# Kernel optimization log

Measured on AMD Instinct MI355X. Metric: run time of the kernel, lower is better.

The kernel has to match this reference:

```python
import jax, jax.numpy as jnp
import numpy as np

D_FEAT = 6
HID = 256
T = 60
B_DAYS = 4
STOCKS = 512
TRAIN_DAYS = 240
K_DAY = 10
N_NEIGHBOR = 10
SLOPE = 0.01  # nn.LeakyReLU default


def setup_inputs() -> dict:
    key = jax.random.key(0)
    ks = jax.random.split(key, 32)
    g = lambda i, shape, s=0.05: (jax.random.normal(ks[i], shape, dtype=jnp.float32) * s)
    inp = jax.random.normal(ks[0], (B_DAYS, STOCKS, D_FEAT * T), dtype=jnp.float32)
    train_hidden = jax.random.normal(ks[1], (TRAIN_DAYS, STOCKS, HID), dtype=jnp.float32)
    train_hidden_day = jax.random.normal(ks[2], (TRAIN_DAYS, HID), dtype=jnp.float32)
    return {
        "inp": inp,
        "train_hidden": train_hidden,
        "train_hidden_day": train_hidden_day,
        # GRU layer 0 (input D_FEAT) and layer 1 (input HID); gates [r,z,n] stacked -> 3*HID
        "W_ih0": g(3, (3 * HID, D_FEAT)), "W_hh0": g(4, (3 * HID, HID)),
        "b_ih0": g(5, (3 * HID,)), "b_hh0": g(6, (3 * HID,)),
        "W_ih1": g(7, (3 * HID, HID)), "W_hh1": g(8, (3 * HID, HID)),
        "b_ih1": g(9, (3 * HID,)), "b_hh1": g(10, (3 * HID,)),
        # lins MLP 256->512->512->256
        "lin0_W": g(11, (512, HID)), "lin0_b": g(12, (512,)),
        "lin1_W": g(13, (512, 512)), "lin1_b": g(14, (512,)),
        "lin2_W": g(15, (HID, 512)), "lin2_b": g(16, (HID,)),
        # projections (no bias) and output head
        "proj1_W": g(17, (HID, HID)), "proj2_W": g(18, (HID, HID)),
        "fc_W": g(19, (1, 2 * HID)), "fc_b": g(20, (1,)),
    }


def _leaky(x):
    return jnp.where(x >= 0, x, SLOPE * x)


def _gru_layer(x, W_ih, W_hh, b_ih, b_hh):
    # x: [N, T, in] -> [N, T, HID]
    xW = jnp.einsum('nti,gi->ntg', x, W_ih) + b_ih  # precompute input gates
    def step(h, xw):
        gh = h @ W_hh.T + b_hh
        xr, xz, xn = jnp.split(xw, 3, axis=-1)
        hr, hz, hn = jnp.split(gh, 3, axis=-1)
        r = jax.nn.sigmoid(xr + hr)
        z = jax.nn.sigmoid(xz + hz)
        n = jnp.tanh(xn + r * hn)
        h = (1.0 - z) * n + z * h
        return h, h
    h0 = jnp.zeros((x.shape[0], W_hh.shape[1]), x.dtype)
    _, hs = jax.lax.scan(step, h0, jnp.swapaxes(xW, 0, 1))
    return jnp.swapaxes(hs, 0, 1)


def _cos_sim(x, y):
    xy = x @ y.T
    xn = jnp.sqrt(jnp.sum(x * x, axis=1))[:, None]
    yn = jnp.sqrt(jnp.sum(y * y, axis=1))[:, None]
    cs = xy / (xn @ yn.T)
    return jnp.where(jnp.isnan(cs), 0.0, cs)


def reference(inp, train_hidden, train_hidden_day,
              W_ih0, W_hh0, b_ih0, b_hh0, W_ih1, W_hh1, b_ih1, b_hh1,
              lin0_W, lin0_b, lin1_W, lin1_b, lin2_W, lin2_b,
              proj1_W, proj2_W, fc_W, fc_b):
    B, S = inp.shape[0], inp.shape[1]
    x = inp.reshape(B * S, D_FEAT, -1).transpose(0, 2, 1)  # [N, T, d_feat]
    h = _gru_layer(x, W_ih0, W_hh0, b_ih0, b_hh0)
    h = _gru_layer(h, W_ih1, W_hh1, b_ih1, b_hh1)
    out = h[:, -1, :]                                      # [N, HID]
    mb = _leaky(out @ lin0_W.T + lin0_b)
    mb = _leaky(mb @ lin1_W.T + lin1_b)
    mb = _leaky(mb @ lin2_W.T + lin2_b)                    # mini_batch_out [N, HID]
    mb_day = jnp.mean(mb.reshape(B, S, -1), axis=1)        # [B, HID]
    day_sim = _cos_sim(mb_day, train_hidden_day)           # [B, TRAIN_DAYS]
    _, day_idx = jax.lax.top_k(day_sim, K_DAY)             # [B, K_DAY]
    sample = train_hidden[day_idx].reshape(-1, train_hidden.shape[-1])  # [B*K_DAY*S, HID]
    q = mb @ proj1_W.T
    kh = sample @ proj2_W.T
    cs = _cos_sim(q, kh)                                   # [N, B*K_DAY*S]
    vals, idx = jax.lax.top_k(cs, N_NEIGHBOR)              # per-row top-k (distinct cols)
    # sparse mask (ones/n_neighbor) * cos_sim, then sparse @ kh == weighted gather-sum
    agg = jnp.einsum('nk,nkh->nh', vals / N_NEIGHBOR, kh[idx])
    cat = jnp.concatenate([mb, agg], axis=1)               # [N, 2*HID]
    y = (cat @ fc_W.T + fc_b).squeeze(-1)
    return y.reshape(B, -1)
```

## Files before the change

### kernel.cpp

```cpp
#include <hip/hip_runtime.h>
#include <cmath>
#include <cstdint>

#define D_FEAT 6
#define T_SEQ  60
#define HID    256
#define G3     768
#define NROW   2048
#define NSAMP  20480

__device__ __forceinline__ float sigmoidf_(float x) { return 1.0f / (1.0f + expf(-x)); }

struct PrepArgs {
  const float* src[9];
  float* dst[9];
  int N[9], K[9], ro[9];
};

__global__ void prep_weights(PrepArgs a) {
  int seg = blockIdx.y;
  const float* S = a.src[seg];
  float* D = a.dst[seg];
  int N = a.N[seg], K = a.K[seg], ro = a.ro[seg];
  int total = N * K;
  for (int i = blockIdx.x * blockDim.x + threadIdx.x; i < total; i += gridDim.x * blockDim.x) {
    int n = i / K, k = i - n * K;
    D[(size_t)(k + ro) * N + n] = S[i];
  }
}

__device__ __forceinline__ void kloop128(const float* __restrict__ A,
                                         const float* __restrict__ B,
                                         float (&acc)[3][8])
{
  float4 Aa[4][2];
  float  Bb[2][12];
#pragma unroll
  for (int c = 0; c < 4; ++c) {
    Aa[c][0] = *(const float4*)(A + c * 8);
    Aa[c][1] = *(const float4*)(A + c * 8 + 4);
  }
#pragma unroll
  for (int c = 0; c < 4; ++c)
#pragma unroll
    for (int u = 0; u < 3; ++u)
      Bb[0][c * 3 + u] = B[(size_t)c * G3 + u * 256];

  for (int kb = 0; kb < 128; kb += 8) {
    {
      const float* p = B + (size_t)(kb + 4) * G3;
#pragma unroll
      for (int c = 0; c < 4; ++c)
#pragma unroll
        for (int u = 0; u < 3; ++u)
          Bb[1][c * 3 + u] = p[(size_t)c * G3 + u * 256];
    }
#pragma unroll
    for (int c = 0; c < 4; ++c) {
      float4 alo = Aa[c][0], ahi = Aa[c][1];
      int kn = kb + 4 + c;
      Aa[c][0] = *(const float4*)(A + kn * 8);
      Aa[c][1] = *(const float4*)(A + kn * 8 + 4);
#pragma unroll
      for (int u = 0; u < 3; ++u) {
        float b = Bb[0][c * 3 + u];
        acc[u][0] += alo.x * b; acc[u][1] += alo.y * b;
        acc[u][2] += alo.z * b; acc[u][3] += alo.w * b;
        acc[u][4] += ahi.x * b; acc[u][5] += ahi.y * b;
        acc[u][6] += ahi.z * b; acc[u][7] += ahi.w * b;
      }
    }
    {
      int kw = (kb + 8) & 127;
      const float* p = B + (size_t)kw * G3;
#pragma unroll
      for (int c = 0; c < 4; ++c)
#pragma unroll
        for (int u = 0; u < 3; ++u)
          Bb[0][c * 3 + u] = p[(size_t)c * G3 + u * 256];
    }
#pragma unroll
    for (int c = 0; c < 4; ++c) {
      float4 alo = Aa[c][0], ahi = Aa[c][1];
      int kn = (kb + 8 + c) & 127;
      Aa[c][0] = *(const float4*)(A + kn * 8);
      Aa[c][1] = *(const float4*)(A + kn * 8 + 4);
#pragma unroll
      for (int u = 0; u < 3; ++u) {
        float b = Bb[1][c * 3 + u];
        acc[u][0] += alo.x * b; acc[u][1] += alo.y * b;
        acc[u][2] += alo.z * b; acc[u][3] += alo.w * b;
        acc[u][4] += ahi.x * b; acc[u][5] += ahi.y * b;
        acc[u][6] += ahi.z * b; acc[u][7] += ahi.w * b;
      }
    }
  }
}

__global__ __launch_bounds__(512, 1)
void gru_fused(const float* __restrict__ inp, const float* __restrict__ WThh0,
               const float* __restrict__ WTcat, const float* __restrict__ WTih0,
               const float* __restrict__ bih0, const float* __restrict__ bhh0,
               const float* __restrict__ bih1, const float* __restrict__ bhh1,
               float* __restrict__ hrow)
{
  __shared__ float h0A[2048], h0B[2048];
  __shared__ float h1A[2048], h1B[2048];
  __shared__ float xls[2880];
  __shared__ float exch[256 * 33];

  const int tid = threadIdx.x;
  const int col = tid & 255;
  const int half = tid >> 8;
  const int m0 = blockIdx.x * 8;

  for (int c = tid; c < 2880; c += 512) {
    int row = c / 360, it = c - row * 360;
    xls[it * 8 + row] = inp[(size_t)(m0 + row) * 360 + it];
  }
  for (int c = tid; c < 2048; c += 512) { h0A[c] = 0.f; h1A[c] = 0.f; }

  float h0c[8], h1c[8];
#pragma unroll
  for (int r = 0; r < 8; ++r) { h0c[r] = 0.f; h1c[r] = 0.f; }

  float b_ih0[3], b_hh0[3], b_ih1[3], b_hh1[3];
#pragma unroll
  for (int u = 0; u < 3; ++u) {
    int o = u * 256 + col;
    b_ih0[u] = bih0[o]; b_hh0[u] = bhh0[o];
    b_ih1[u] = bih1[o]; b_hh1[u] = bhh1[o];
  }
  __syncthreads();

  const int aoff = half * 1024;
  const float* Bhh0 = WThh0 + (size_t)(half * 128) * G3 + col;
  const float* Bc0  = WTcat + (size_t)(half * 128) * G3 + col;
  const float* Bc1  = WTcat + (size_t)(256 + half * 128) * G3 + col;
  float* exc = exch + col * 33;

  for (int t = 0; t < T_SEQ; ++t) {
    const float* h0cur = (t & 1) ? h0B : h0A;
    float*       h0nxt = (t & 1) ? h0A : h0B;
    const float* h1cur = (t & 1) ? h1B : h1A;
    float*       h1nxt = (t & 1) ? h1A : h1B;

    float gh[3][8];
#pragma unroll
    for (int u = 0; u < 3; ++u)
#pragma unroll
      for (int r = 0; r < 8; ++r) gh[u][r] = 0.f;
    kloop128(h0cur + aoff, Bhh0, gh);

    float xw[3][8];
    if (half == 0) {
#pragma unroll
      for (int u = 0; u < 3; ++u)
#pragma unroll
        for (int r = 0; r < 8; ++r) xw[u][r] = b_ih0[u];
#pragma unroll
      for (int i = 0; i < 6; ++i) {
        float4 xlo = *(const float4*)&xls[(i * 60 + t) * 8];
        float4 xhi = *(const float4*)&xls[(i * 60 + t) * 8 + 4];
#pragma unroll
        for (int u = 0; u < 3; ++u) {
          float b = WTih0[i * G3 + u * 256 + col];
          xw[u][0] += xlo.x * b; xw[u][1] += xlo.y * b;
          xw[u][2] += xlo.z * b; xw[u][3] += xlo.w * b;
          xw[u][4] += xhi.x * b; xw[u][5] += xhi.y * b;
          xw[u][6] += xhi.z * b; xw[u][7] += xhi.w * b;
        }
      }
    } else {
#pragma unroll
      for (int u = 0; u < 3; ++u)
#pragma unroll
        for (int r = 0; r < 8; ++r) exc[u * 8 + r] = gh[u][r];
    }
    __syncthreads();

    if (half == 0) {
      float hn[8];
#pragma unroll
      for (int r = 0; r < 8; ++r) {
        float g0 = gh[0][r] + exc[r];
        float g1 = gh[1][r] + exc[8 + r];
        float g2 = gh[2][r] + exc[16 + r];
        float rr = sigmoidf_(xw[0][r] + (g0 + b_hh0[0]));
        float zz = sigmoidf_(xw[1][r] + (g1 + b_hh0[1]));
        float nn = tanhf(xw[2][r] + rr * (g2 + b_hh0[2]));
        h0c[r] = (1.f - zz) * nn + zz * h0c[r];
        hn[r] = h0c[r];
      }
      *(float4*)&h0nxt[col * 8]     = *(float4*)&hn[0];
      *(float4*)&h0nxt[col * 8 + 4] = *(float4*)&hn[4];
    }
    __syncthreads();

    float acc[3][8];
#pragma unroll
    for (int u = 0; u < 3; ++u)
#pragma unroll
      for (int r = 0; r < 8; ++r) acc[u][r] = 0.f;
    kloop128(h0nxt + aoff, Bc0, acc);
    float xn8[8];
#pragma unroll
    for (int r = 0; r < 8; ++r) { xn8[r] = acc[2][r]; acc[2][r] = 0.f; }
    kloop128(h1cur + aoff, Bc1, acc);

    if (half == 1) {
#pragma unroll
      for (int r = 0; r < 8; ++r) {
        exc[r]      = acc[0][r];
        exc[8 + r]  = acc[1][r];
        exc[16 + r] = xn8[r];
        exc[24 + r] = acc[2][r];
      }
    }
    __syncthreads();

    if (half == 0) {
      float hn[8];
#pragma unroll
      for (int r = 0; r < 8; ++r) {
        float ra = acc[0][r] + exc[r];
        float za = acc[1][r] + exc[8 + r];
        float xa = xn8[r] + exc[16 + r];
        float ha = acc[2][r] + exc[24 + r];
        float rr = sigmoidf_((ra + b_ih1[0]) + b_hh1[0]);
        float zz = sigmoidf_((za + b_ih1[1]) + b_hh1[1]);
        float nn = tanhf((xa + b_ih1[2]) + rr * (ha + b_hh1[2]));
        h1c[r] = (1.f - zz) * nn + zz * h1c[r];
        hn[r] = h1c[r];
      }
      *(float4*)&h1nxt[col * 8]     = *(float4*)&hn[0];
      *(float4*)&h1nxt[col * 8 + 4] = *(float4*)&hn[4];
    }
    __syncthreads();
  }

  if (half == 0) {
#pragma unroll
    for (int r = 0; r < 8; ++r)
      hrow[(size_t)(m0 + r) * 256 + col] = h1c[r];
  }
}

__global__ __launch_bounds__(256, 2)
void gemm_act(const float* __restrict__ A, const int* __restrict__ rowsrc,
              const float* __restrict__ WT, const float* __restrict__ bias,
              float* __restrict__ C, int M, int N, int K, int act)
{
  __shared__ float4 As4[128 * 32];
  const int tx = threadIdx.x, ty = threadIdx.y;
  const int tid = ty * 32 + tx;
  const int n0 = blockIdx.x * 32, m0 = blockIdx.y * 32;
  const int K4 = K >> 2;

  for (int c = tid; c < K4 * 32; c += 256) {
    int k4 = c % K4, m = c / K4;
    int row = m0 + m;
    if (rowsrc) row = rowsrc[row];
    As4[k4 * 32 + m] = *(const float4*)(A + (size_t)row * K + k4 * 4);
  }
  __syncthreads();

  float acc[4] = {0,0,0,0};
  const int n = n0 + tx;
  const float* pb = WT + n;

  float bc[4], bn_[4];
#pragma unroll
  for (int kk = 0; kk < 4; ++kk) bc[kk] = pb[(size_t)kk * N];
  for (int k4 = 0; k4 < K4; ++k4) {
    int nk4 = (k4 + 1 < K4) ? (k4 + 1) : 0;
    const float* pn = pb + (size_t)nk4 * 4 * N;
#pragma unroll
    for (int kk = 0; kk < 4; ++kk) bn_[kk] = pn[(size_t)kk * N];
    float4 a0 = As4[k4 * 32 + ty * 4 + 0];
    float4 a1 = As4[k4 * 32 + ty * 4 + 1];
    float4 a2 = As4[k4 * 32 + ty * 4 + 2];
    float4 a3 = As4[k4 * 32 + ty * 4 + 3];
#pragma unroll
    for (int kk = 0; kk < 4; ++kk) {
      float b = bc[kk];
      acc[0] += ((const float*)&a0)[kk] * b;
      acc[1] += ((const float*)&a1)[kk] * b;
      acc[2] += ((const float*)&a2)[kk] * b;
      acc[3] += ((const float*)&a3)[kk] * b;
    }
#pragma unroll
    for (int q = 0; q < 4; ++q) bc[q] = bn_[q];
  }
  float bb = bias ? bias[n] : 0.f;
#pragma unroll
  for (int r = 0; r < 4; ++r) {
    float v = acc[r] + bb;
    if (act) v = (v >= 0.f) ? v : 0.01f * v;
    C[(size_t)(m0 + ty * 4 + r) * N + n] = v;
  }
}

__global__ void mbday_part(const float* __restrict__ mbf, float* __restrict__ part) {
  int d = blockIdx.x, sl = blockIdx.y, c = threadIdx.x;
  float s = 0.f;
  int base = d * 512 + sl * 64;
  for (int st = 0; st < 64; ++st) s += mbf[(size_t)(base + st) * 256 + c];
  part[(size_t)(d * 8 + sl) * 256 + c] = s;
}

__global__ void mbday_fin(const float* __restrict__ part, float* __restrict__ mbday) {
  int d = blockIdx.x, c = threadIdx.x;
  float s = 0.f;
#pragma unroll
  for (int p = 0; p < 8; ++p) s += part[(size_t)(d * 8 + p) * 256 + c];
  mbday[d * 256 + c] = s * (1.0f / 512.0f);
}

__global__ void daytopk_kernel(const float* __restrict__ mbday, const float* __restrict__ thd,
                               int* __restrict__ dayidx) {
  __shared__ float mbs[256];
  __shared__ float sim[256];
  __shared__ float red[256];
  __shared__ int   redi[256];
  const int d = blockIdx.x, t = threadIdx.x;
  mbs[t] = mbday[d * 256 + t];
  __syncthreads();
  red[t] = mbs[t] * mbs[t];
  __syncthreads();
  for (int o = 128; o; o >>= 1) { if (t < o) red[t] += red[t + o]; __syncthreads(); }
  float xn = sqrtf(red[0]);
  float v = -INFINITY;
  if (t < 240) {
    float dot = 0.f, yn2 = 0.f;
    for (int k = 0; k < 256; ++k) {
      float y = thd[t * 256 + k];
      dot += mbs[k] * y;
      yn2 += y * y;
    }
    float den = xn * sqrtf(yn2);
    v = (den > 0.f) ? dot / den : 0.f;
  }
  sim[t] = v;
  __syncthreads();
  for (int it = 0; it < 10; ++it) {
    red[t] = sim[t]; redi[t] = t;
    __syncthreads();
    for (int o = 128; o; o >>= 1) {
      if (t < o) {
        if (red[t + o] > red[t] || (red[t + o] == red[t] && redi[t + o] < redi[t])) {
          red[t] = red[t + o]; redi[t] = redi[t + o];
        }
      }
      __syncthreads();
    }
    if (t == 0) { int bi = redi[0]; dayidx[d * 10 + it] = bi; sim[bi] = -INFINITY; }
    __syncthreads();
  }
}

__global__ void rowsrc_kernel(const int* __restrict__ dayidx, int* __restrict__ rowsrc) {
  int r = blockIdx.x * 256 + threadIdx.x;
  if (r < NSAMP) rowsrc[r] = dayidx[r >> 9] * 512 + (r & 511);
}

__global__ void rownorm_kernel(const float* __restrict__ X, float* __restrict__ out, int rows) {
  int w = threadIdx.x >> 6;
  int lane = threadIdx.x & 63;
  int row = blockIdx.x * 4 + w;
  if (row >= rows) return;
  float4 x = *(const float4*)(X + (size_t)row * 256 + lane * 4);
  float s = x.x * x.x + x.y * x.y + x.z * x.z + x.w * x.w;
#pragma unroll
  for (int o = 32; o; o >>= 1) s += __shfl_down(s, o, 64);
  if (lane == 0) out[row] = sqrtf(s);
}

__global__ void qnorm_kernel(float* __restrict__ q, const float* __restrict__ qn) {
  int i = blockIdx.x * 256 + threadIdx.x;
  int row = i >> 8;
  float n = qn[row];
  q[i] = (n > 0.f) ? q[i] / n : 0.f;
}

__global__ void khT_kernel(const float* __restrict__ kh, const float* __restrict__ khn,
                           float* __restrict__ khT) {
  __shared__ float tile[32][33];
  int jb = blockIdx.x * 32;
  int kb = blockIdx.y * 32;
  int tx = threadIdx.x & 31, tyy = threadIdx.x >> 5;
  for (int rr = tyy; rr < 32; rr += 8) {
    float n = khn[jb + rr];
    float v = kh[(size_t)(jb + rr) * 256 + kb + tx];
    tile[rr][tx] = (n > 0.f) ? v / n : 0.f;
  }
  __syncthreads();
  for (int rr = tyy; rr < 32; rr += 8) {
    khT[(size_t)(kb + rr) * NSAMP + jb + tx] = tile[tx][rr];
  }
}

__global__ __launch_bounds__(256, 4)
void csmax_kernel(const float* __restrict__ qh, const float* __restrict__ khT,
                  float* __restrict__ topvp, int* __restrict__ topip)
{
  __shared__ float4 qs[256][2];
  __shared__ float csch[8 * 512];
  const int tid = threadIdx.x;
  const int split = blockIdx.x & 7;
  const int m0 = (blockIdx.x >> 3) * 8;
  {
    int k = tid;
    float4 v0, v1;
    v0.x = qh[(size_t)(m0 + 0) * 256 + k]; v0.y = qh[(size_t)(m0 + 1) * 256 + k];
    v0.z = qh[(size_t)(m0 + 2) * 256 + k]; v0.w = qh[(size_t)(m0 + 3) * 256 + k];
    v1.x = qh[(size_t)(m0 + 4) * 256 + k]; v1.y = qh[(size_t)(m0 + 5) * 256 + k];
    v1.z = qh[(size_t)(m0 + 6) * 256 + k]; v1.w = qh[(size_t)(m0 + 7) * 256 + k];
    qs[k][0] = v0; qs[k][1] = v1;
  }
  __syncthreads();
  const int lane = tid & 63;
  const int wv = tid >> 6;

  float tv0[10], tv1[10];
  int   tj0[10], tj1[10];
  int   tn0 = 0, tn1 = 0;
  float tmv0 = -INFINITY, tmv1 = -INFINITY;
  int   tmi0 = 0, tmi1 = 0;

  auto process_row = [&](int r, float (&tv)[10], int (&tj)[10], int& tn,
                         float& tmv, int& tmi, int jb) {
    float4 c0 = *(const float4*)&csch[r * 512 + lane * 8];
    float4 c1 = *(const float4*)&csch[r * 512 + lane * 8 + 4];
    float cv[8] = {c0.x, c0.y, c0.z, c0.w, c1.x, c1.y, c1.z, c1.w};
    const int cj0 = jb + lane * 8;
    while (true) {
      float bv = -INFINITY; int bj = 0x7fffffff;
#pragma unroll
      for (int u = 0; u < 8; ++u) {
        if (cv[u] > bv) { bv = cv[u]; bj = cj0 + u; }
      }
#pragma unroll
      for (int o = 32; o; o >>= 1) {
        float ov = __shfl_down(bv, o, 64);
        int   oj = __shfl_down(bj, o, 64);
        if (ov > bv || (ov == bv && oj < bj)) { bv = ov; bj = oj; }
      }
      bv = __shfl(bv, 0, 64); bj = __shfl(bj, 0, 64);
      bool take;
      if (tn < 10) take = true;
      else take = (bv > tmv) || (bv == tmv && bj < tmi);
      if (!take) break;
      if (tn < 10) {
#pragma unroll
        for (int s = 0; s < 10; ++s) if (s == tn) { tv[s] = bv; tj[s] = bj; }
        tn++;
        if (tn == 10) {
          float mv = tv[0]; int mi = tj[0];
#pragma unroll
          for (int s = 1; s < 10; ++s) {
            bool w = (tv[s] < mv) || (tv[s] == mv && tj[s] > mi);
            if (w) { mv = tv[s]; mi = tj[s]; }
          }
          tmv = mv; tmi = mi;
        }
      } else {
        int ms = 0; float mv = tv[0]; int mi = tj[0];
#pragma unroll
        for (int s = 1; s < 10; ++s) {
          bool w = (tv[s] < mv) || (tv[s] == mv && tj[s] > mi);
          if (w) { ms = s; mv = tv[s]; mi = tj[s]; }
        }
#pragma unroll
        for (int s = 0; s < 10; ++s) if (s == ms) { tv[s] = bv; tj[s] = bj; }
        mv = tv[0]; mi = tj[0];
#pragma unroll
        for (int s = 1; s < 10; ++s) {
          bool w = (tv[s] < mv) || (tv[s] == mv && tj[s] > mi);
          if (w) { mv = tv[s]; mi = tj[s]; }
        }
        tmv = mv; tmi = mi;
      }
#pragma unroll
      for (int u = 0; u < 8; ++u) if (cj0 + u == bj) cv[u] = -INFINITY;
    }
  };

  for (int ci = 0; ci < 5; ++ci) {
    const int ch = split * 5 + ci;
    const int jb = ch * 512;
    float acc[8][2];
#pragma unroll
    for (int r = 0; r < 8; ++r) { acc[r][0] = 0.f; acc[r][1] = 0.f; }
    const float* kp = khT + jb + tid;

    float b0c[4], b1c[4], b0n[4], b1n[4];
#pragma unroll
    for (int kk = 0; kk < 4; ++kk) {
      b0c[kk] = kp[(size_t)kk * NSAMP];
      b1c[kk] = kp[(size_t)kk * NSAMP + 256];
    }
    for (int k4 = 0; k4 < 64; ++k4) {
      int nk4 = (k4 + 1) & 63;
      const float* pn = kp + (size_t)nk4 * 4 * NSAMP;
#pragma unroll
      for (int kk = 0; kk < 4; ++kk) {
        b0n[kk] = pn[(size_t)kk * NSAMP];
        b1n[kk] = pn[(size_t)kk * NSAMP + 256];
      }
#pragma unroll
      for (int kk = 0; kk < 4; ++kk) {
        float4 qa = qs[k4 * 4 + kk][0];
        float4 qb = qs[k4 * 4 + kk][1];
        float b0 = b0c[kk], b1 = b1c[kk];
        acc[0][0] += qa.x * b0; acc[1][0] += qa.y * b0; acc[2][0] += qa.z * b0; acc[3][0] += qa.w * b0;
        acc[4][0] += qb.x * b0; acc[5][0] += qb.y * b0; acc[6][0] += qb.z * b0; acc[7][0] += qb.w * b0;
        acc[0][1] += qa.x * b1; acc[1][1] += qa.y * b1; acc[2][1] += qa.z * b1; acc[3][1] += qa.w * b1;
        acc[4][1] += qb.x * b1; acc[5][1] += qb.y * b1; acc[6][1] += qb.z * b1; acc[7][1] += qb.w * b1;
      }
#pragma unroll
      for (int q = 0; q < 4; ++q) { b0c[q] = b0n[q]; b1c[q] = b1n[q]; }
    }
    __syncthreads();
#pragma unroll
    for (int r = 0; r < 8; ++r) {
      csch[r * 512 + tid] = acc[r][0];
      csch[r * 512 + 256 + tid] = acc[r][1];
    }
    __syncthreads();
    process_row(wv,     tv0, tj0, tn0, tmv0, tmi0, jb);
    process_row(wv + 4, tv1, tj1, tn1, tmv1, tmi1, jb);
  }
  __syncthreads();

  if (lane == 0) {
    int row0 = m0 + wv;
#pragma unroll
    for (int s = 0; s < 10; ++s) {
      topvp[(size_t)row0 * 80 + split * 10 + s] = tv0[s];
      topip[(size_t)row0 * 80 + split * 10 + s] = tj0[s];
    }
    int row1 = m0 + wv + 4;
#pragma unroll
    for (int s = 0; s < 10; ++s) {
      topvp[(size_t)row1 * 80 + split * 10 + s] = tv1[s];
      topip[(size_t)row1 * 80 + split * 10 + s] = tj1[s];
    }
  }
}

__global__ void merge_topk(const float* __restrict__ topvp, const int* __restrict__ topip,
                           float* __restrict__ topv, int* __restrict__ topi)
{
  const int wv = threadIdx.x >> 6;
  const int lane = threadIdx.x & 63;
  const int row = blockIdx.x * 4 + wv;
  float v0 = topvp[(size_t)row * 80 + lane];
  int   i0 = topip[(size_t)row * 80 + lane];
  float v1 = (lane < 16) ? topvp[(size_t)row * 80 + 64 + lane] : -INFINITY;
  int   i1 = (lane < 16) ? topip[(size_t)row * 80 + 64 + lane] : 0x7fffffff;
  for (int s = 0; s < 10; ++s) {
    float bv = v0; int bj = i0;
    if (v1 > bv || (v1 == bv && i1 < bj)) { bv = v1; bj = i1; }
#pragma unroll
    for (int o = 1; o < 64; o <<= 1) {
      float ov = __shfl_xor(bv, o, 64);
      int   oj = __shfl_xor(bj, o, 64);
      if (ov > bv || (ov == bv && oj < bj)) { bv = ov; bj = oj; }
    }
    if (lane == 0) { topv[row * 10 + s] = bv; topi[row * 10 + s] = bj; }
    if (i0 == bj) { v0 = -INFINITY; i0 = 0x7fffffff; }
    if (i1 == bj) { v1 = -INFINITY; i1 = 0x7fffffff; }
  }
}

__global__ void final_kernel(const float* __restrict__ mb, const float* __restrict__ kh,
                             const float* __restrict__ topv, const int* __restrict__ topi,
                             const float* __restrict__ fcW, const float* __restrict__ fcb,
                             float* __restrict__ y)
{
  __shared__ float red[256];
  int n = blockIdx.x, c = threadIdx.x;
  float agg = 0.f;
#pragma unroll
  for (int k = 0; k < 10; ++k) {
    float w = topv[n * 10 + k] / 10.0f;
    int idx = topi[n * 10 + k];
    agg += w * kh[(size_t)idx * 256 + c];
  }
  float val = fcW[c] * mb[(size_t)n * 256 + c] + fcW[256 + c] * agg;
  red[c] = val;
  __syncthreads();
  for (int o = 128; o; o >>= 1) { if (c < o) red[c] += red[c + o]; __syncthreads(); }
  if (c == 0) y[n] = red[0] + fcb[0];
}

extern "C" void kernel_launch(void* const* d_in, const int* in_sizes, int n_in,
                              void* d_out, int out_size, void* d_ws, size_t ws_size,
                              hipStream_t stream)
{
  const float* inp    = (const float*)d_in[0];
  const float* trainh = (const float*)d_in[1];
  const float* thd    = (const float*)d_in[2];
  const float* Wih0   = (const float*)d_in[3];
  const float* Whh0   = (const float*)d_in[4];
  const float* bih0   = (const float*)d_in[5];
  const float* bhh0   = (const float*)d_in[6];
  const float* Wih1   = (const float*)d_in[7];
  const float* Whh1   = (const float*)d_in[8];
  const float* bih1   = (const float*)d_in[9];
  const float* bhh1   = (const float*)d_in[10];
  const float* lin0W  = (const float*)d_in[11];
  const float* lin0b  = (const float*)d_in[12];
  const float* lin1W  = (const float*)d_in[13];
  const float* lin1b  = (const float*)d_in[14];
  const float* lin2W  = (const float*)d_in[15];
  const float* lin2b  = (const float*)d_in[16];
  const float* p1W    = (const float*)d_in[17];
  const float* p2W    = (const float*)d_in[18];
  const float* fcW    = (const float*)d_in[19];
  const float* fcb    = (const float*)d_in[20];

  float* ws = (float*)d_ws;
  float* WT_hh0 = ws + 0;
  float* WTcat  = ws + 196608;
  float* WT_l0  = ws + 589824;
  float* WT_l1  = ws + 720896;
  float* WT_l2  = ws + 983040;
  float* WT_p1  = ws + 1114112;
  float* WT_p2  = ws + 1179648;
  float* hrow   = ws + 1245184;
  float* mb1    = ws + 3342336;
  float* mb2    = ws + 4390912;
  float* mbf    = ws + 5439488;
  float* mbday  = ws + 5963776;
  float* qbuf   = ws + 5964800;
  float* kh     = ws + 6489088;
  float* khT    = ws + 11731968;
  float* khn    = ws + 16974848;
  float* qn     = ws + 16995328;
  float* topv   = ws + 16997376;
  int*   dayidx = (int*)(ws + 17017856);
  int*   rowsrc = (int*)(ws + 17017920);
  int*   topi   = (int*)(ws + 17038400);
  float* topvp  = mb1;
  int*   topip  = (int*)(mb1 + 163840);
  float* WT_ih0 = mb2;
  float* mbpart = mb2;

  PrepArgs pa;
  pa.src[0] = Whh0;  pa.dst[0] = WT_hh0; pa.N[0] = 768; pa.K[0] = 256; pa.ro[0] = 0;
  pa.src[1] = Wih1;  pa.dst[1] = WTcat;  pa.N[1] = 768; pa.K[1] = 256; pa.ro[1] = 0;
  pa.src[2] = Whh1;  pa.dst[2] = WTcat;  pa.N[2] = 768; pa.K[2] = 256; pa.ro[2] = 256;
  pa.src[3] = lin0W; pa.dst[3] = WT_l0;  pa.N[3] = 512; pa.K[3] = 256; pa.ro[3] = 0;
  pa.src[4] = lin1W; pa.dst[4] = WT_l1;  pa.N[4] = 512; pa.K[4] = 512; pa.ro[4] = 0;
  pa.src[5] = lin2W; pa.dst[5] = WT_l2;  pa.N[5] = 256; pa.K[5] = 512; pa.ro[5] = 0;
  pa.src[6] = p1W;   pa.dst[6] = WT_p1;  pa.N[6] = 256; pa.K[6] = 256; pa.ro[6] = 0;
  pa.src[7] = p2W;   pa.dst[7] = WT_p2;  pa.N[7] = 256; pa.K[7] = 256; pa.ro[7] = 0;
  pa.src[8] = Wih0;  pa.dst[8] = WT_ih0; pa.N[8] = 768; pa.K[8] = 6;   pa.ro[8] = 0;
  prep_weights<<<dim3(64, 9), dim3(256), 0, stream>>>(pa);

  gru_fused<<<256, 512, 0, stream>>>(inp, WT_hh0, WTcat, WT_ih0, bih0, bhh0, bih1, bhh1, hrow);

  gemm_act<<<dim3(16, 64), dim3(32, 8), 0, stream>>>(hrow, nullptr, WT_l0, lin0b, mb1, 2048, 512, 256, 1);
  gemm_act<<<dim3(16, 64), dim3(32, 8), 0, stream>>>(mb1, nullptr, WT_l1, lin1b, mb2, 2048, 512, 512, 1);
  gemm_act<<<dim3(8, 64),  dim3(32, 8), 0, stream>>>(mb2, nullptr, WT_l2, lin2b, mbf, 2048, 256, 512, 1);

  mbday_part<<<dim3(4, 8), 256, 0, stream>>>(mbf, mbpart);
  mbday_fin<<<4, 256, 0, stream>>>(mbpart, mbday);
  daytopk_kernel<<<4, 256, 0, stream>>>(mbday, thd, dayidx);
  rowsrc_kernel<<<80, 256, 0, stream>>>(dayidx, rowsrc);

  gemm_act<<<dim3(8, 640), dim3(32, 8), 0, stream>>>(trainh, rowsrc, WT_p2, nullptr, kh, 20480, 256, 256, 0);
  gemm_act<<<dim3(8, 64),  dim3(32, 8), 0, stream>>>(mbf, nullptr, WT_p1, nullptr, qbuf, 2048, 256, 256, 0);

  rownorm_kernel<<<5120, 256, 0, stream>>>(kh, khn, 20480);
  rownorm_kernel<<<512, 256, 0, stream>>>(qbuf, qn, 2048);
  qnorm_kernel<<<2048, 256, 0, stream>>>(qbuf, qn);
  khT_kernel<<<dim3(640, 8), 256, 0, stream>>>(kh, khn, khT);

  csmax_kernel<<<2048, 256, 0, stream>>>(qbuf, khT, topvp, topip);
  merge_topk<<<512, 256, 0, stream>>>(topvp, topip, topv, topi);
  final_kernel<<<2048, 256, 0, stream>>>(mbf, kh, topv, topi, fcW, fcb, (float*)d_out);

  (void)in_sizes; (void)n_in; (void)out_size; (void)ws_size;
}
```

Before: 3.283 ms.

## Pipeline GRU layers across timesteps and split rows over 1024 threads

The fused two-layer GRU kernel now runs layer 0 at step p and layer 1 at step p-1 in the same phase. This drops one of the two barriers per step and lets all three k-loops run concurrently. The block grows to 1024 threads, with each thread covering 4 rows instead of 8, so per-thread registers drop and more waves are available to hide latency. The cost is that each weight column is read twice per block from global memory/cache, and there is one extra pipeline step at the end.

```diff
diff --git a/kernel.cpp b/kernel.cpp
--- a/kernel.cpp
+++ b/kernel.cpp
@@ -29,17 +29,14 @@
   }
 }
 
-__device__ __forceinline__ void kloop128(const float* __restrict__ A,
-                                         const float* __restrict__ B,
-                                         float (&acc)[3][8])
+__device__ __forceinline__ void kloop128q(const float* __restrict__ A,
+                                          const float* __restrict__ B,
+                                          float (&acc)[3][4])
 {
-  float4 Aa[4][2];
+  float4 Aa[4];
   float  Bb[2][12];
 #pragma unroll
-  for (int c = 0; c < 4; ++c) {
-    Aa[c][0] = *(const float4*)(A + c * 8);
-    Aa[c][1] = *(const float4*)(A + c * 8 + 4);
-  }
+  for (int c = 0; c < 4; ++c) Aa[c] = *(const float4*)(A + c * 8);
 #pragma unroll
   for (int c = 0; c < 4; ++c)
 #pragma unroll
@@ -57,17 +54,14 @@
     }
 #pragma unroll
     for (int c = 0; c < 4; ++c) {
-      float4 alo = Aa[c][0], ahi = Aa[c][1];
+      float4 a = Aa[c];
       int kn = kb + 4 + c;
-      Aa[c][0] = *(const float4*)(A + kn * 8);
-      Aa[c][1] = *(const float4*)(A + kn * 8 + 4);
+      Aa[c] = *(const float4*)(A + kn * 8);
 #pragma unroll
       for (int u = 0; u < 3; ++u) {
         float b = Bb[0][c * 3 + u];
-        acc[u][0] += alo.x * b; acc[u][1] += alo.y * b;
-        acc[u][2] += alo.z * b; acc[u][3] += alo.w * b;
-        acc[u][4] += ahi.x * b; acc[u][5] += ahi.y * b;
-        acc[u][6] += ahi.z * b; acc[u][7] += ahi.w * b;
+        acc[u][0] += a.x * b; acc[u][1] += a.y * b;
+        acc[u][2] += a.z * b; acc[u][3] += a.w * b;
       }
     }
     {
@@ -81,48 +75,46 @@
     }
 #pragma unroll
     for (int c = 0; c < 4; ++c) {
-      float4 alo = Aa[c][0], ahi = Aa[c][1];
+      float4 a = Aa[c];
       int kn = (kb + 8 + c) & 127;
-      Aa[c][0] = *(const float4*)(A + kn * 8);
-      Aa[c][1] = *(const float4*)(A + kn * 8 + 4);
+      Aa[c] = *(const float4*)(A + kn * 8);
 #pragma unroll
       for (int u = 0; u < 3; ++u) {
         float b = Bb[1][c * 3 + u];
-        acc[u][0] += alo.x * b; acc[u][1] += alo.y * b;
-        acc[u][2] += alo.z * b; acc[u][3] += alo.w * b;
-        acc[u][4] += ahi.x * b; acc[u][5] += ahi.y * b;
-        acc[u][6] += ahi.z * b; acc[u][7] += ahi.w * b;
-      }
-    }
-  }
-}
-
-__global__ __launch_bounds__(512, 1)
-void gru_fused(const float* __restrict__ inp, const float* __restrict__ WThh0,
-               const float* __restrict__ WTcat, const float* __restrict__ WTih0,
-               const float* __restrict__ bih0, const float* __restrict__ bhh0,
-               const float* __restrict__ bih1, const float* __restrict__ bhh1,
-               float* __restrict__ hrow)
+        acc[u][0] += a.x * b; acc[u][1] += a.y * b;
+        acc[u][2] += a.z * b; acc[u][3] += a.w * b;
+      }
+    }
+  }
+}
+
+__global__ __launch_bounds__(1024, 1)
+void gru_pipe(const float* __restrict__ inp, const float* __restrict__ WThh0,
+              const float* __restrict__ WTcat, const float* __restrict__ WTih0,
+              const float* __restrict__ bih0, const float* __restrict__ bhh0,
+              const float* __restrict__ bih1, const float* __restrict__ bhh1,
+              float* __restrict__ hrow)
 {
   __shared__ float h0A[2048], h0B[2048];
   __shared__ float h1A[2048], h1B[2048];
   __shared__ float xls[2880];
-  __shared__ float exch[256 * 33];
+  __shared__ float exch[512 * 29];
 
   const int tid = threadIdx.x;
   const int col = tid & 255;
-  const int half = tid >> 8;
+  const int sub = tid >> 8;
+  const int khalf = sub & 1;
+  const int mhalf = sub >> 1;
   const int m0 = blockIdx.x * 8;
-
-  for (int c = tid; c < 2880; c += 512) {
+  const int aoff = khalf * 1024 + mhalf * 4;
+
+  for (int c = tid; c < 2880; c += 1024) {
     int row = c / 360, it = c - row * 360;
     xls[it * 8 + row] = inp[(size_t)(m0 + row) * 360 + it];
   }
-  for (int c = tid; c < 2048; c += 512) { h0A[c] = 0.f; h1A[c] = 0.f; }
-
-  float h0c[8], h1c[8];
-#pragma unroll
-  for (int r = 0; r < 8; ++r) { h0c[r] = 0.f; h1c[r] = 0.f; }
+  for (int c = tid; c < 2048; c += 1024) { h0A[c] = 0.f; h1B[c] = 0.f; }
+
+  float h0c[4] = {0,0,0,0}, h1c[4] = {0,0,0,0};
 
   float b_ih0[3], b_hh0[3], b_ih1[3], b_hh1[3];
 #pragma unroll
@@ -133,116 +125,116 @@
   }
   __syncthreads();
 
-  const int aoff = half * 1024;
-  const float* Bhh0 = WThh0 + (size_t)(half * 128) * G3 + col;
-  const float* Bc0  = WTcat + (size_t)(half * 128) * G3 + col;
-  const float* Bc1  = WTcat + (size_t)(256 + half * 128) * G3 + col;
-  float* exc = exch + col * 33;
-
-  for (int t = 0; t < T_SEQ; ++t) {
-    const float* h0cur = (t & 1) ? h0B : h0A;
-    float*       h0nxt = (t & 1) ? h0A : h0B;
-    const float* h1cur = (t & 1) ? h1B : h1A;
-    float*       h1nxt = (t & 1) ? h1A : h1B;
-
-    float gh[3][8];
-#pragma unroll
-    for (int u = 0; u < 3; ++u)
-#pragma unroll
-      for (int r = 0; r < 8; ++r) gh[u][r] = 0.f;
-    kloop128(h0cur + aoff, Bhh0, gh);
-
-    float xw[3][8];
-    if (half == 0) {
+  const float* Bhh0 = WThh0 + (size_t)(khalf * 128) * G3 + col;
+  const float* Bc0  = WTcat + (size_t)(khalf * 128) * G3 + col;
+  const float* Bc1  = WTcat + (size_t)(256 + khalf * 128) * G3 + col;
+  float* exc = exch + (col * 2 + mhalf) * 29;
+
+  for (int p = 0; p <= 60; ++p) {
+    const float* h0cur = (p & 1) ? h0B : h0A;
+    float*       h0nxt = (p & 1) ? h0A : h0B;
+    const float* h1cur = (p & 1) ? h1B : h1A;
+    float*       h1nxt = (p & 1) ? h1A : h1B;
+
+    float gh[3][4];
+    float l1[3][4];
+    float xn4[4];
+    if (p < 60) {
 #pragma unroll
       for (int u = 0; u < 3; ++u)
 #pragma unroll
-        for (int r = 0; r < 8; ++r) xw[u][r] = b_ih0[u];
+        for (int r = 0; r < 4; ++r) gh[u][r] = 0.f;
+      kloop128q(h0cur + aoff, Bhh0, gh);
+    }
+    if (p > 0) {
+#pragma unroll
+      for (int u = 0; u < 3; ++u)
+#pragma unroll
+        for (int r = 0; r < 4; ++r) l1[u][r] = 0.f;
+      kloop128q(h0cur + aoff, Bc0, l1);
+#pragma unroll
+      for (int r = 0; r < 4; ++r) { xn4[r] = l1[2][r]; l1[2][r] = 0.f; }
+      kloop128q(h1cur + aoff, Bc1, l1);
+    }
+
+    float xw[3][4];
+    if (khalf == 1) {
+      if (p < 60) {
+#pragma unroll
+        for (int u = 0; u < 3; ++u)
+#pragma unroll
+          for (int r = 0; r < 4; ++r) exc[u * 4 + r] = gh[u][r];
+      }
+      if (p > 0) {
+#pragma unroll
+        for (int r = 0; r < 4; ++r) {
+          exc[12 + r] = l1[0][r];
+          exc[16 + r] = l1[1][r];
+          exc[20 + r] = xn4[r];
+          exc[24 + r] = l1[2][r];
+        }
+      }
+    } else if (p < 60) {
+#pragma unroll
+      for (int u = 0; u < 3; ++u)
+#pragma unroll
+        for (int r = 0; r < 4; ++r) xw[u][r] = b_ih0[u];
 #pragma unroll
       for (int i = 0; i < 6; ++i) {
-        float4 xlo = *(const float4*)&xls[(i * 60 + t) * 8];
-        float4 xhi = *(const float4*)&xls[(i * 60 + t) * 8 + 4];
+        float x0 = xls[(i * 60 + p) * 8 + mhalf * 4 + 0];
+        float x1 = xls[(i * 60 + p) * 8 + mhalf * 4 + 1];
+        float x2 = xls[(i * 60 + p) * 8 + mhalf * 4 + 2];
+        float x3 = xls[(i * 60 + p) * 8 + mhalf * 4 + 3];
 #pragma unroll
         for (int u = 0; u < 3; ++u) {
           float b = WTih0[i * G3 + u * 256 + col];
-          xw[u][0] += xlo.x * b; xw[u][1] += xlo.y * b;
-          xw[u][2] += xlo.z * b; xw[u][3] += xlo.w * b;
-          xw[u][4] += xhi.x * b; xw[u][5] += xhi.y * b;
-          xw[u][6] += xhi.z * b; xw[u][7] += xhi.w * b;
-        }
-      }
-    } else {
-#pragma unroll
-      for (int u = 0; u < 3; ++u)
-#pragma unroll
-        for (int r = 0; r < 8; ++r) exc[u * 8 + r] = gh[u][r];
+          xw[u][0] += x0 * b; xw[u][1] += x1 * b;
+          xw[u][2] += x2 * b; xw[u][3] += x3 * b;
+        }
+      }
     }
     __syncthreads();
 
-    if (half == 0) {
-      float hn[8];
-#pragma unroll
-      for (int r = 0; r < 8; ++r) {
-        float g0 = gh[0][r] + exc[r];
-        float g1 = gh[1][r] + exc[8 + r];
-        float g2 = gh[2][r] + exc[16 + r];
-        float rr = sigmoidf_(xw[0][r] + (g0 + b_hh0[0]));
-        float zz = sigmoidf_(xw[1][r] + (g1 + b_hh0[1]));
-        float nn = tanhf(xw[2][r] + rr * (g2 + b_hh0[2]));
-        h0c[r] = (1.f - zz) * nn + zz * h0c[r];
-        hn[r] = h0c[r];
-      }
-      *(float4*)&h0nxt[col * 8]     = *(float4*)&hn[0];
-      *(float4*)&h0nxt[col * 8 + 4] = *(float4*)&hn[4];
+    if (khalf == 0) {
+      if (p < 60) {
+        float hn[4];
+#pragma unroll
+        for (int r = 0; r < 4; ++r) {
+          float g0 = gh[0][r] + exc[r];
+          float g1 = gh[1][r] + exc[4 + r];
+          float g2 = gh[2][r] + exc[8 + r];
+          float rr = sigmoidf_(xw[0][r] + (g0 + b_hh0[0]));
+          float zz = sigmoidf_(xw[1][r] + (g1 + b_hh0[1]));
+          float nn = tanhf(xw[2][r] + rr * (g2 + b_hh0[2]));
+          h0c[r] = (1.f - zz) * nn + zz * h0c[r];
+          hn[r] = h0c[r];
+        }
+        *(float4*)&h0nxt[col * 8 + mhalf * 4] = *(float4*)hn;
+      }
+      if (p > 0) {
+        float hn[4];
+#pragma unroll
+        for (int r = 0; r < 4; ++r) {
+          float ra = l1[0][r] + exc[12 + r];
+          float za = l1[1][r] + exc[16 + r];
+          float xa = xn4[r] + exc[20 + r];
+          float ha = l1[2][r] + exc[24 + r];
+          float rr = sigmoidf_((ra + b_ih1[0]) + b_hh1[0]);
+          float zz = sigmoidf_((za + b_ih1[1]) + b_hh1[1]);
+          float nn = tanhf((xa + b_ih1[2]) + rr * (ha + b_hh1[2]));
+          h1c[r] = (1.f - zz) * nn + zz * h1c[r];
+          hn[r] = h1c[r];
+        }
+        *(float4*)&h1nxt[col * 8 + mhalf * 4] = *(float4*)hn;
+      }
     }
     __syncthreads();
-
-    float acc[3][8];
-#pragma unroll
-    for (int u = 0; u < 3; ++u)
-#pragma unroll
-      for (int r = 0; r < 8; ++r) acc[u][r] = 0.f;
-    kloop128(h0nxt + aoff, Bc0, acc);
-    float xn8[8];
-#pragma unroll
-    for (int r = 0; r < 8; ++r) { xn8[r] = acc[2][r]; acc[2][r] = 0.f; }
-    kloop128(h1cur + aoff, Bc1, acc);
-
-    if (half == 1) {
-#pragma unroll
-      for (int r = 0; r < 8; ++r) {
-        exc[r]      = acc[0][r];
-        exc[8 + r]  = acc[1][r];
-        exc[16 + r] = xn8[r];
-        exc[24 + r] = acc[2][r];
-      }
-    }
-    __syncthreads();
-
-    if (half == 0) {
-      float hn[8];
-#pragma unroll
-      for (int r = 0; r < 8; ++r) {
-        float ra = acc[0][r] + exc[r];
-        float za = acc[1][r] + exc[8 + r];
-        float xa = xn8[r] + exc[16 + r];
-        float ha = acc[2][r] + exc[24 + r];
-        float rr = sigmoidf_((ra + b_ih1[0]) + b_hh1[0]);
-        float zz = sigmoidf_((za + b_ih1[1]) + b_hh1[1]);
-        float nn = tanhf((xa + b_ih1[2]) + rr * (ha + b_hh1[2]));
-        h1c[r] = (1.f - zz) * nn + zz * h1c[r];
-        hn[r] = h1c[r];
-      }
-      *(float4*)&h1nxt[col * 8]     = *(float4*)&hn[0];
-      *(float4*)&h1nxt[col * 8 + 4] = *(float4*)&hn[4];
-    }
-    __syncthreads();
-  }
-
-  if (half == 0) {
-#pragma unroll
-    for (int r = 0; r < 8; ++r)
-      hrow[(size_t)(m0 + r) * 256 + col] = h1c[r];
+  }
+
+  if (khalf == 0) {
+#pragma unroll
+    for (int r = 0; r < 4; ++r)
+      hrow[(size_t)(m0 + mhalf * 4 + r) * 256 + col] = h1c[r];
   }
 }
 
@@ -660,7 +652,7 @@
   pa.src[8] = Wih0;  pa.dst[8] = WT_ih0; pa.N[8] = 768; pa.K[8] = 6;   pa.ro[8] = 0;
   prep_weights<<<dim3(64, 9), dim3(256), 0, stream>>>(pa);
 
-  gru_fused<<<256, 512, 0, stream>>>(inp, WT_hh0, WTcat, WT_ih0, bih0, bhh0, bih1, bhh1, hrow);
+  gru_pipe<<<256, 1024, 0, stream>>>(inp, WT_hh0, WTcat, WT_ih0, bih0, bhh0, bih1, bhh1, hrow);
 
   gemm_act<<<dim3(16, 64), dim3(32, 8), 0, stream>>>(hrow, nullptr, WT_l0, lin0b, mb1, 2048, 512, 256, 1);
   gemm_act<<<dim3(16, 64), dim3(32, 8), 0, stream>>>(mb1, nullptr, WT_l1, lin1b, mb2, 2048, 512, 512, 1);
```

After: 4.652 ms. +41.7%, slower.

## Wavefront-pipeline GRU layers so layer 1 step t overlaps layer 0 step t+1

Applied to the files above, without the earlier changes.

The two-layer GRU recurrence is skewed so each iteration computes layer 0 for step p and layer 1 for step p-1 together. The two thread halves split the epilogues, with half 0 updating layer 0 and half 1 updating layer 1. This cuts the barriers per step from four to two and runs both layers' matvec work in the same phase. It adds a second exchange buffer in shared memory, one extra pipeline iteration, and more live registers per thread.

```diff
diff --git a/kernel.cpp b/kernel.cpp
--- a/kernel.cpp
+++ b/kernel.cpp
@@ -98,31 +98,32 @@
 }
 
 __global__ __launch_bounds__(512, 1)
-void gru_fused(const float* __restrict__ inp, const float* __restrict__ WThh0,
-               const float* __restrict__ WTcat, const float* __restrict__ WTih0,
-               const float* __restrict__ bih0, const float* __restrict__ bhh0,
-               const float* __restrict__ bih1, const float* __restrict__ bhh1,
-               float* __restrict__ hrow)
+void gru_pipe(const float* __restrict__ inp, const float* __restrict__ WThh0,
+              const float* __restrict__ WTcat, const float* __restrict__ WTih0,
+              const float* __restrict__ bih0, const float* __restrict__ bhh0,
+              const float* __restrict__ bih1, const float* __restrict__ bhh1,
+              float* __restrict__ hrow)
 {
   __shared__ float h0A[2048], h0B[2048];
   __shared__ float h1A[2048], h1B[2048];
   __shared__ float xls[2880];
-  __shared__ float exch[256 * 33];
+  __shared__ float excA[256 * 33];
+  __shared__ float excB[256 * 25];
 
   const int tid = threadIdx.x;
   const int col = tid & 255;
-  const int half = tid >> 8;
+  const int khalf = tid >> 8;
   const int m0 = blockIdx.x * 8;
+  const int aoff = khalf * 1024;
 
   for (int c = tid; c < 2880; c += 512) {
     int row = c / 360, it = c - row * 360;
     xls[it * 8 + row] = inp[(size_t)(m0 + row) * 360 + it];
   }
-  for (int c = tid; c < 2048; c += 512) { h0A[c] = 0.f; h1A[c] = 0.f; }
-
-  float h0c[8], h1c[8];
-#pragma unroll
-  for (int r = 0; r < 8; ++r) { h0c[r] = 0.f; h1c[r] = 0.f; }
+  for (int c = tid; c < 2048; c += 512) { h0A[c] = 0.f; h1B[c] = 0.f; }
+
+  float h0c[8] = {0,0,0,0,0,0,0,0};
+  float h1c[8] = {0,0,0,0,0,0,0,0};
 
   float b_ih0[3], b_hh0[3], b_ih1[3], b_hh1[3];
 #pragma unroll
@@ -133,113 +134,129 @@
   }
   __syncthreads();
 
-  const int aoff = half * 1024;
-  const float* Bhh0 = WThh0 + (size_t)(half * 128) * G3 + col;
-  const float* Bc0  = WTcat + (size_t)(half * 128) * G3 + col;
-  const float* Bc1  = WTcat + (size_t)(256 + half * 128) * G3 + col;
-  float* exc = exch + col * 33;
-
-  for (int t = 0; t < T_SEQ; ++t) {
-    const float* h0cur = (t & 1) ? h0B : h0A;
-    float*       h0nxt = (t & 1) ? h0A : h0B;
-    const float* h1cur = (t & 1) ? h1B : h1A;
-    float*       h1nxt = (t & 1) ? h1A : h1B;
+  const float* Bhh0 = WThh0 + (size_t)(khalf * 128) * G3 + col;
+  const float* Bc0  = WTcat + (size_t)(khalf * 128) * G3 + col;
+  const float* Bc1  = WTcat + (size_t)(256 + khalf * 128) * G3 + col;
+  float* eA = excA + col * 33;
+  float* eB = excB + col * 25;
+
+  for (int p = 0; p <= 60; ++p) {
+    const float* h0cur = (p & 1) ? h0B : h0A;
+    float*       h0nxt = (p & 1) ? h0A : h0B;
+    const float* h1cur = (p & 1) ? h1B : h1A;
+    float*       h1nxt = (p & 1) ? h1A : h1B;
 
     float gh[3][8];
-#pragma unroll
-    for (int u = 0; u < 3; ++u)
-#pragma unroll
-      for (int r = 0; r < 8; ++r) gh[u][r] = 0.f;
-    kloop128(h0cur + aoff, Bhh0, gh);
-
+    float l1[3][8], xn8[8];
     float xw[3][8];
-    if (half == 0) {
-#pragma unroll
-      for (int u = 0; u < 3; ++u)
-#pragma unroll
-        for (int r = 0; r < 8; ++r) xw[u][r] = b_ih0[u];
-#pragma unroll
-      for (int i = 0; i < 6; ++i) {
-        float4 xlo = *(const float4*)&xls[(i * 60 + t) * 8];
-        float4 xhi = *(const float4*)&xls[(i * 60 + t) * 8 + 4];
-#pragma unroll
-        for (int u = 0; u < 3; ++u) {
-          float b = WTih0[i * G3 + u * 256 + col];
-          xw[u][0] += xlo.x * b; xw[u][1] += xlo.y * b;
-          xw[u][2] += xlo.z * b; xw[u][3] += xlo.w * b;
-          xw[u][4] += xhi.x * b; xw[u][5] += xhi.y * b;
-          xw[u][6] += xhi.z * b; xw[u][7] += xhi.w * b;
+
+    if (khalf == 1) {
+      if (p < 60) {
+#pragma unroll
+        for (int u = 0; u < 3; ++u)
+#pragma unroll
+          for (int r = 0; r < 8; ++r) gh[u][r] = 0.f;
+        kloop128(h0cur + aoff, Bhh0, gh);
+#pragma unroll
+        for (int u = 0; u < 3; ++u)
+#pragma unroll
+          for (int r = 0; r < 8; ++r) eB[u * 8 + r] = gh[u][r];
+      }
+      if (p > 0) {
+#pragma unroll
+        for (int u = 0; u < 3; ++u)
+#pragma unroll
+          for (int r = 0; r < 8; ++r) l1[u][r] = 0.f;
+        kloop128(h0cur + aoff, Bc0, l1);
+#pragma unroll
+        for (int r = 0; r < 8; ++r) { xn8[r] = l1[2][r]; l1[2][r] = 0.f; }
+        kloop128(h1cur + aoff, Bc1, l1);
+      }
+    } else {
+      if (p > 0) {
+#pragma unroll
+        for (int u = 0; u < 3; ++u)
+#pragma unroll
+          for (int r = 0; r < 8; ++r) l1[u][r] = 0.f;
+        kloop128(h0cur + aoff, Bc0, l1);
+#pragma unroll
+        for (int r = 0; r < 8; ++r) { xn8[r] = l1[2][r]; l1[2][r] = 0.f; }
+        kloop128(h1cur + aoff, Bc1, l1);
+#pragma unroll
+        for (int r = 0; r < 8; ++r) {
+          eA[r]      = l1[0][r];
+          eA[8 + r]  = l1[1][r];
+          eA[16 + r] = xn8[r];
+          eA[24 + r] = l1[2][r];
         }
       }
+      if (p < 60) {
+#pragma unroll
+        for (int u = 0; u < 3; ++u)
+#pragma unroll
+          for (int r = 0; r < 8; ++r) gh[u][r] = 0.f;
+        kloop128(h0cur + aoff, Bhh0, gh);
+#pragma unroll
+        for (int u = 0; u < 3; ++u)
+#pragma unroll
+          for (int r = 0; r < 8; ++r) xw[u][r] = b_ih0[u];
+#pragma unroll
+        for (int i = 0; i < 6; ++i) {
+          float4 xlo = *(const float4*)&xls[(i * 60 + p) * 8];
+          float4 xhi = *(const float4*)&xls[(i * 60 + p) * 8 + 4];
+#pragma unroll
+          for (int u = 0; u < 3; ++u) {
+            float b = WTih0[i * G3 + u * 256 + col];
+            xw[u][0] += xlo.x * b; xw[u][1] += xlo.y * b;
+            xw[u][2] += xlo.z * b; xw[u][3] += xlo.w * b;
+            xw[u][4] += xhi.x * b; xw[u][5] += xhi.y * b;
+            xw[u][6] += xhi.z * b; xw[u][7] += xhi.w * b;
+          }
+        }
+      }
+    }
+    __syncthreads();
+
+    if (khalf == 0) {
+      if (p < 60) {
+        float hn[8];
+#pragma unroll
+        for (int r = 0; r < 8; ++r) {
+          float g0 = gh[0][r] + eB[r];
+          float g1 = gh[1][r] + eB[8 + r];
+          float g2 = gh[2][r] + eB[16 + r];
+          float rr = sigmoidf_(xw[0][r] + (g0 + b_hh0[0]));
+          float zz = sigmoidf_(xw[1][r] + (g1 + b_hh0[1]));
+          float nn = tanhf(xw[2][r] + rr * (g2 + b_hh0[2]));
+          h0c[r] = (1.f - zz) * nn + zz * h0c[r];
+          hn[r] = h0c[r];
+        }
+        *(float4*)&h0nxt[col * 8]     = *(float4*)&hn[0];
+        *(float4*)&h0nxt[col * 8 + 4] = *(float4*)&hn[4];
+      }
     } else {
-#pragma unroll
-      for (int u = 0; u < 3; ++u)
-#pragma unroll
-        for (int r = 0; r < 8; ++r) exc[u * 8 + r] = gh[u][r];
+      if (p > 0) {
+        float hn[8];
+#pragma unroll
+        for (int r = 0; r < 8; ++r) {
+          float ra = eA[r]      + l1[0][r];
+          float za = eA[8 + r]  + l1[1][r];
+          float xa = eA[16 + r] + xn8[r];
+          float ha = eA[24 + r] + l1[2][r];
+          float rr = sigmoidf_((ra + b_ih1[0]) + b_hh1[0]);
+          float zz = sigmoidf_((za + b_ih1[1]) + b_hh1[1]);
+          float nn = tanhf((xa + b_ih1[2]) + rr * (ha + b_hh1[2]));
+          h1c[r] = (1.f - zz) * nn + zz * h1c[r];
+          hn[r] = h1c[r];
+        }
+        *(float4*)&h1nxt[col * 8]     = *(float4*)&hn[0];
+        *(float4*)&h1nxt[col * 8 + 4] = *(float4*)&hn[4];
+      }
     }
     __syncthreads();
-
-    if (half == 0) {
-      float hn[8];
-#pragma unroll
-      for (int r = 0; r < 8; ++r) {
-        float g0 = gh[0][r] + exc[r];
-        float g1 = gh[1][r] + exc[8 + r];
-        float g2 = gh[2][r] + exc[16 + r];
-        float rr = sigmoidf_(xw[0][r] + (g0 + b_hh0[0]));
-        float zz = sigmoidf_(xw[1][r] + (g1 + b_hh0[1]));
-        float nn = tanhf(xw[2][r] + rr * (g2 + b_hh0[2]));
-        h0c[r] = (1.f - zz) * nn + zz * h0c[r];
-        hn[r] = h0c[r];
-      }
-      *(float4*)&h0nxt[col * 8]     = *(float4*)&hn[0];
-      *(float4*)&h0nxt[col * 8 + 4] = *(float4*)&hn[4];
-    }
-    __syncthreads();
-
-    float acc[3][8];
-#pragma unroll
-    for (int u = 0; u < 3; ++u)
-#pragma unroll
-      for (int r = 0; r < 8; ++r) acc[u][r] = 0.f;
-    kloop128(h0nxt + aoff, Bc0, acc);
-    float xn8[8];
-#pragma unroll
-    for (int r = 0; r < 8; ++r) { xn8[r] = acc[2][r]; acc[2][r] = 0.f; }
-    kloop128(h1cur + aoff, Bc1, acc);
-
-    if (half == 1) {
-#pragma unroll
-      for (int r = 0; r < 8; ++r) {
-        exc[r]      = acc[0][r];
-        exc[8 + r]  = acc[1][r];
-        exc[16 + r] = xn8[r];
-        exc[24 + r] = acc[2][r];
-      }
-    }
-    __syncthreads();
-
-    if (half == 0) {
-      float hn[8];
-#pragma unroll
-      for (int r = 0; r < 8; ++r) {
-        float ra = acc[0][r] + exc[r];
-        float za = acc[1][r] + exc[8 + r];
-        float xa = xn8[r] + exc[16 + r];
-        float ha = acc[2][r] + exc[24 + r];
-        float rr = sigmoidf_((ra + b_ih1[0]) + b_hh1[0]);
-        float zz = sigmoidf_((za + b_ih1[1]) + b_hh1[1]);
-        float nn = tanhf((xa + b_ih1[2]) + rr * (ha + b_hh1[2]));
-        h1c[r] = (1.f - zz) * nn + zz * h1c[r];
-        hn[r] = h1c[r];
-      }
-      *(float4*)&h1nxt[col * 8]     = *(float4*)&hn[0];
-      *(float4*)&h1nxt[col * 8 + 4] = *(float4*)&hn[4];
-    }
-    __syncthreads();
-  }
-
-  if (half == 0) {
+  }
+
+  if (khalf == 1) {
 #pragma unroll
     for (int r = 0; r < 8; ++r)
       hrow[(size_t)(m0 + r) * 256 + col] = h1c[r];
@@ -660,7 +677,7 @@
   pa.src[8] = Wih0;  pa.dst[8] = WT_ih0; pa.N[8] = 768; pa.K[8] = 6;   pa.ro[8] = 0;
   prep_weights<<<dim3(64, 9), dim3(256), 0, stream>>>(pa);
 
-  gru_fused<<<256, 512, 0, stream>>>(inp, WT_hh0, WTcat, WT_ih0, bih0, bhh0, bih1, bhh1, hrow);
+  gru_pipe<<<256, 512, 0, stream>>>(inp, WT_hh0, WTcat, WT_ih0, bih0, bhh0, bih1, bhh1, hrow);
 
   gemm_act<<<dim3(16, 64), dim3(32, 8), 0, stream>>>(hrow, nullptr, WT_l0, lin0b, mb1, 2048, 512, 256, 1);
   gemm_act<<<dim3(16, 64), dim3(32, 8), 0, stream>>>(mb1, nullptr, WT_l1, lin1b, mb2, 2048, 512, 512, 1);
```

Result: slower. 3.624 ms (+10.4%).
